# Optimization experiments

Measured on AMD Instinct MI355X. Metric: run time of the kernel, lower is better.

## Reference

```python
import jax, jax.numpy as jnp
import numpy as np

EPS = 1e-5
TAU = 0.5
K = 1024  # number of gumbel-softmax iterations


def _bn(x, gamma, beta):
    # BatchNorm1d, training semantics: batch mean, biased variance
    mean = jnp.mean(x, axis=0)
    var = jnp.mean(jnp.square(x - mean), axis=0)
    xn = (x - mean) * jax.lax.rsqrt(var + EPS)
    if gamma is None:
        return xn
    return xn * gamma + beta


def setup_inputs() -> dict:
    key = jax.random.key(0)
    ks = jax.random.split(key, 5)
    B, D, M = 64, 2048, 8192
    f = jax.random.normal(ks[0], (B, D), jnp.float32)
    W1 = jax.random.normal(ks[1], (D, M), jnp.float32) * 0.02
    b1 = jnp.zeros((M,), jnp.float32)
    g1 = jnp.ones((M,), jnp.float32)
    be1 = jnp.zeros((M,), jnp.float32)
    W2 = jax.random.normal(ks[2], (M, M), jnp.float32) * 0.02
    b2 = jnp.zeros((M,), jnp.float32)
    g2 = jnp.ones((M,), jnp.float32)
    be2 = jnp.zeros((M,), jnp.float32)
    W3 = jax.random.normal(ks[3], (M, D), jnp.float32) * 0.02
    b3 = jnp.zeros((D,), jnp.float32)
    return dict(f=f, W1=W1, b1=b1, g1=g1, be1=be1,
                W2=W2, b2=b2, g2=g2, be2=be2, W3=W3, b3=b3)


def reference(f, W1, b1, g1, be1, W2, b2, g2, be2, W3, b3):
    # MLP trunk (dropout layers are identity in eval mode)
    h = jax.nn.relu(_bn(f @ W1 + b1, g1, be1))
    h = jax.nn.relu(_bn(h @ W2 + b2, g2, be2))
    mask0 = _bn(h @ W3 + b3, None, None)  # final BN, affine=False

    noise_key = jax.random.key(42)

    def step(carry, i):
        mask, z = carry
        g = jax.random.gumbel(jax.random.fold_in(noise_key, i),
                              mask.shape, mask.dtype)
        mask = jax.nn.softmax((mask + g) / TAU, axis=1)
        z = jnp.maximum(mask, z)
        return (mask, z), None

    (_, z), _ = jax.lax.scan(step, (mask0, jnp.zeros_like(mask0)),
                             jnp.arange(K))
    return z
```

## Files before the change

kernel.cpp:

```cpp
#include <hip/hip_runtime.h>


typedef _Float16 half8 __attribute__((ext_vector_type(8)));
typedef float floatx4 __attribute__((ext_vector_type(4)));

#define TINYF 1.17549435e-38f
#define LN2F  0.69314718055994531f
#define C2F   2.8853900817779268f
#define TSCALE 512.0f
#define TS_MIN 6.11e-5f

#define COMBINE(o0, o1) ((o0) ^ (o1))

#if __has_builtin(__builtin_amdgcn_exp2f)
#define EXP2F(x) __builtin_amdgcn_exp2f(x)
#else
#define EXP2F(x) exp2f(x)
#endif
#if __has_builtin(__builtin_amdgcn_logf)
#define LOG2F(x) __builtin_amdgcn_logf(x)
#else
#define LOG2F(x) __log2f(x)
#endif
#if __has_builtin(__builtin_amdgcn_rcpf)
#define RCPF(x) __builtin_amdgcn_rcpf(x)
#else
#define RCPF(x) (1.0f/(x))
#endif

__device__ __forceinline__ unsigned rotl32(unsigned x, int r) {
  return (x << r) | (x >> (32 - r));
}

__device__ __forceinline__ void tf2x32(unsigned k0, unsigned k1,
                                       unsigned x0, unsigned x1,
                                       unsigned &o0, unsigned &o1) {
  unsigned kx = k0 ^ k1 ^ 0x1BD11BDAu;
#define TFR(r) { x0 += x1; x1 = rotl32(x1, (r)); x1 ^= x0; }
  x0 += k0; x1 += k1;
  TFR(13) TFR(15) TFR(26) TFR(6)
  x0 += k1; x1 += kx + 1u;
  TFR(17) TFR(29) TFR(16) TFR(24)
  x0 += kx; x1 += k0 + 2u;
  TFR(13) TFR(15) TFR(26) TFR(6)
  x0 += k0; x1 += k1 + 3u;
  TFR(17) TFR(29) TFR(16) TFR(24)
  x0 += k1; x1 += kx + 4u;
  TFR(13) TFR(15) TFR(26) TFR(6)
  x0 += kx; x1 += k0 + 5u;
#undef TFR
  o0 = x0; o1 = x1;
}

__device__ __forceinline__ float bits_to_t(unsigned bits) {
  float f = __uint_as_float((bits >> 9) | 0x3f800000u) - 1.0f;
  float u = fmaxf(TINYF, f + TINYF);
  return fmaxf(-LN2F * LOG2F(u), 1.0e-7f);
}

__device__ __forceinline__ float wave_sum64(float x) {
  x += __int_as_float(__builtin_amdgcn_update_dpp(0, __float_as_int(x), 0xB1, 0xF, 0xF, true));
  x += __int_as_float(__builtin_amdgcn_update_dpp(0, __float_as_int(x), 0x4E, 0xF, 0xF, true));
  x += __int_as_float(__builtin_amdgcn_update_dpp(0, __float_as_int(x), 0x141, 0xF, 0xF, true));
  x += __int_as_float(__builtin_amdgcn_update_dpp(0, __float_as_int(x), 0x140, 0xF, 0xF, true));
  x += __int_as_float(__builtin_amdgcn_update_dpp(0, __float_as_int(x), 0x142, 0xA, 0xF, true));
  x += __int_as_float(__builtin_amdgcn_update_dpp(0, __float_as_int(x), 0x143, 0xC, 0xF, true));
  return __int_as_float(__builtin_amdgcn_readlane(__float_as_int(x), 63));
}

__global__ void keys_kernel(unsigned* __restrict__ keys) {
  int i = threadIdx.x;
  unsigned o0, o1;
  tf2x32(0u, 42u, 0u, (unsigned)i, o0, o1);
  keys[2*i] = o0; keys[2*i+1] = o1;
}

__global__ void cast_kernel(const float* __restrict__ f, _Float16* __restrict__ o) {
  int i = blockIdx.x * 256 + threadIdx.x;
  o[i] = (_Float16)f[i];
}

__global__ __launch_bounds__(256) void gemm_kernel(
    const _Float16* __restrict__ A, const float* __restrict__ W,
    float* __restrict__ P, int K, int N, int KC) {
  __shared__ _Float16 As[64 * 40];
  __shared__ _Float16 Ws[128 * 40];
  const int t = threadIdx.x;
  const int lane = t & 63, w = t >> 6;
  const int c0 = blockIdx.x * 128;
  const int k0beg = blockIdx.y * KC, k0end = k0beg + KC;

  floatx4 acc[4][2];
#pragma unroll
  for (int i = 0; i < 4; ++i)
#pragma unroll
    for (int j = 0; j < 2; ++j) acc[i][j] = (floatx4){0.f, 0.f, 0.f, 0.f};

  const int ar = t >> 2;
  const int ako = (t & 3) * 8;
  const int wn = (t & 31) * 4;
  const int wk = (t >> 5) * 2;

  uint4 av = *(const uint4*)(A + (size_t)ar * K + k0beg + ako);
  float4 wv[2][2];
#pragma unroll
  for (int kk = 0; kk < 2; ++kk) {
    int krow = k0beg + kk * 16 + wk;
    wv[kk][0] = *(const float4*)(W + (size_t)krow * N + c0 + wn);
    wv[kk][1] = *(const float4*)(W + (size_t)(krow + 1) * N + c0 + wn);
  }

  for (int k0 = k0beg; k0 < k0end; k0 += 32) {
    __syncthreads();
    *(uint4*)(&As[ar * 40 + ako]) = av;
#pragma unroll
    for (int kk = 0; kk < 2; ++kk) {
#pragma unroll
      for (int i = 0; i < 4; ++i) {
        const float* p0 = (const float*)&wv[kk][0];
        const float* p1 = (const float*)&wv[kk][1];
        _Float16 h0 = (_Float16)p0[i], h1 = (_Float16)p1[i];
        unsigned u = (unsigned)*(unsigned short*)&h0 |
                     ((unsigned)*(unsigned short*)&h1 << 16);
        *(unsigned*)(&Ws[(wn + i) * 40 + kk * 16 + wk]) = u;
      }
    }
    int kn = k0 + 32;
    if (kn < k0end) {
      av = *(const uint4*)(A + (size_t)ar * K + kn + ako);
#pragma unroll
      for (int kk = 0; kk < 2; ++kk) {
        int krow = kn + kk * 16 + wk;
        wv[kk][0] = *(const float4*)(W + (size_t)krow * N + c0 + wn);
        wv[kk][1] = *(const float4*)(W + (size_t)(krow + 1) * N + c0 + wn);
      }
    }
    __syncthreads();
    const int q = lane >> 4, ml = lane & 15;
    half8 bfrag[2];
#pragma unroll
    for (int nt = 0; nt < 2; ++nt)
      bfrag[nt] = *(const half8*)(&Ws[(w * 32 + nt * 16 + ml) * 40 + q * 8]);
#pragma unroll
    for (int mt = 0; mt < 4; ++mt) {
      half8 afrag = *(const half8*)(&As[(mt * 16 + ml) * 40 + q * 8]);
      acc[mt][0] = __builtin_amdgcn_mfma_f32_16x16x32_f16(afrag, bfrag[0], acc[mt][0], 0, 0, 0);
      acc[mt][1] = __builtin_amdgcn_mfma_f32_16x16x32_f16(afrag, bfrag[1], acc[mt][1], 0, 0, 0);
    }
  }
  const int q = lane >> 4, ml = lane & 15;
  float* Pb = P + (size_t)blockIdx.y * 64 * N;
#pragma unroll
  for (int mt = 0; mt < 4; ++mt)
#pragma unroll
    for (int nt = 0; nt < 2; ++nt)
#pragma unroll
      for (int i = 0; i < 4; ++i) {
        int m = mt * 16 + q * 4 + i;
        int n = c0 + w * 32 + nt * 16 + ml;
        Pb[(size_t)m * N + n] = acc[mt][nt][i];
      }
}

__global__ __launch_bounds__(256) void reduce_kernel(
    const float* __restrict__ P, float* __restrict__ X, int nkc, int total) {
  int i = blockIdx.x * 256 + threadIdx.x;
  float s = 0.f;
  for (int kc = 0; kc < nkc; ++kc) s += P[(size_t)kc * total + i];
  X[i] = s;
}

__global__ __launch_bounds__(256) void bn_kernel(
    const float* __restrict__ P, int nkc, int N,
    const float* __restrict__ g, const float* __restrict__ be,
    _Float16* __restrict__ Hout, float* __restrict__ Fout, int mode) {
  int c = blockIdx.x * 256 + threadIdx.x;
  float x[64];
#pragma unroll
  for (int r = 0; r < 64; ++r) x[r] = 0.f;
  for (int kc = 0; kc < nkc; ++kc) {
    const float* Pb = P + (size_t)kc * 64 * N + c;
#pragma unroll
    for (int r = 0; r < 64; ++r) x[r] += Pb[(size_t)r * N];
  }
  float s = 0.f;
#pragma unroll
  for (int r = 0; r < 64; ++r) s += x[r];
  float mean = s * 0.015625f;
  float v = 0.f;
#pragma unroll
  for (int r = 0; r < 64; ++r) { float d = x[r] - mean; v += d * d; }
  v *= 0.015625f;
  float rs = rsqrtf(v + 1e-5f);
  if (mode == 0) {
    float gg = g[c], bb = be[c];
#pragma unroll
    for (int r = 0; r < 64; ++r) {
      float y = (x[r] - mean) * rs * gg + bb;
      Hout[(size_t)r * N + c] = (_Float16)fmaxf(y, 0.f);
    }
  } else {
#pragma unroll
    for (int r = 0; r < 64; ++r)
      Fout[(size_t)r * N + c] = (x[r] - mean) * rs;
  }
}

__global__ __launch_bounds__(256) void noise_kernel(
    const unsigned* __restrict__ keys, _Float16* __restrict__ noise) {
  const int bx = blockIdx.x;
  const int r = bx & 63, sg = bx >> 6;
  const int t = threadIdx.x;
  union Pack { unsigned v[16]; unsigned short us[32]; } pa;
#pragma unroll
  for (int j = 0; j < 4; ++j) {
    unsigned kk0 = keys[(sg * 4 + j) * 2];
    unsigned kk1 = keys[(sg * 4 + j) * 2 + 1];
#pragma unroll
    for (int q = 0; q < 8; ++q) {
      unsigned x1 = (unsigned)(r * 2048 + t * 8 + q);
      unsigned o0, o1;
      tf2x32(kk0, kk1, 0u, x1, o0, o1);
      float ts = fmaxf(bits_to_t(COMBINE(o0, o1)) * TSCALE, TS_MIN);
      _Float16 h = (_Float16)ts;
      pa.us[q * 4 + j] = *(unsigned short*)&h;
    }
  }
  size_t base = (((size_t)r * 256 + sg) * 2048 + (size_t)t * 8) * 4;
  uint4* wp = (uint4*)(noise + base);
#pragma unroll
  for (int i = 0; i < 4; ++i) wp[i] = ((uint4*)pa.v)[i];
}

template <int MODE>
__global__ __launch_bounds__(256) void loop_kernel(
    const float* __restrict__ mask0, const _Float16* __restrict__ noise,
    const unsigned* __restrict__ keys, float* __restrict__ zout) {
  const int row = blockIdx.x;
  const int t = threadIdx.x;
  const int lane = t & 63, w = t >> 6;
  __shared__ __align__(16) float partial[2][4];
  __shared__ unsigned keysLds[2048];

  float p[8], z[8];
  {
    union { float4 v[2]; float f[8]; } mm;
    mm.v[0] = *(const float4*)(mask0 + row * 2048 + t * 8);
    mm.v[1] = *(const float4*)(mask0 + row * 2048 + t * 8 + 4);
#pragma unroll
    for (int q = 0; q < 8; ++q) { p[q] = mm.f[q]; z[q] = 0.f; }
  }

  if (MODE == 0) {
    const _Float16* nbase = noise + (size_t)row * 2097152;
    float aC = C2F;
    float lgA[8][4], lgB[8][4];
    uint4 nbufA[4], nbufB[4];

    auto prep8 = [&](float (&LN)[8][4], const uint4 (&nbC)[4], int j) {
#pragma unroll
      for (int q = 0; q < 8; ++q) {
        int h = q * 4 + j;
        unsigned d = ((const unsigned*)&nbC[h >> 3])[(h >> 1) & 3];
        unsigned short usv = (h & 1) ? (unsigned short)(d >> 16)
                                     : (unsigned short)(d & 0xffffu);
        _Float16 hv;
        __builtin_memcpy(&hv, &usv, 2);
        LN[q][j] = -2.0f * LOG2F((float)hv);
      }
    };

    {
      uint4 nbI[4];
      const uint4* p0 = (const uint4*)(nbase + (size_t)t * 32);
      nbI[0] = p0[0]; nbI[1] = p0[1]; nbI[2] = p0[2]; nbI[3] = p0[3];
#pragma unroll
      for (int j = 0; j < 4; ++j) prep8(lgA, nbI, j);
      const uint4* p1 = (const uint4*)(nbase + 8192 + (size_t)t * 32);
      nbufA[0] = p1[0]; nbufA[1] = p1[1]; nbufA[2] = p1[2]; nbufA[3] = p1[3];
    }

    auto run_group = [&](const float (&LC)[8][4], float (&LN)[8][4],
                         const uint4 (&nbC)[4], uint4 (&nbL)[4], int sg) {
      int gl = (sg + 2 < 256) ? sg + 2 : 255;
      const uint4* pl = (const uint4*)(nbase + (size_t)gl * 8192 + (size_t)t * 32);
      nbL[0] = pl[0]; nbL[1] = pl[1]; nbL[2] = pl[2]; nbL[3] = pl[3];
#pragma unroll
      for (int j = 0; j < 4; ++j) {
        float pn[8];
#pragma unroll
        for (int q = 0; q < 8; ++q)
          pn[q] = EXP2F(fmaf(p[q], aC, LC[q][j]));
        float s = ((pn[0] + pn[1]) + (pn[2] + pn[3])) +
                  ((pn[4] + pn[5]) + (pn[6] + pn[7]));
        s = wave_sum64(s);
        if (lane == 0) partial[j & 1][w] = s;
        __syncthreads();
        float4 ps = *(const float4*)(&partial[j & 1][0]);
        prep8(LN, nbC, j);
        float S = (ps.x + ps.y) + (ps.z + ps.w);
        float inv = RCPF(S);
        aC = inv * C2F;
#pragma unroll
        for (int q = 0; q < 8; ++q) {
          z[q] = fmaxf(z[q], pn[q] * inv);
          p[q] = pn[q];
        }
      }
    };

    for (int sgp = 0; sgp < 128; ++sgp) {
      run_group(lgA, lgB, nbufA, nbufB, 2 * sgp);
      run_group(lgB, lgA, nbufB, nbufA, 2 * sgp + 1);
    }
  } else {
    for (int i = t; i < 2048; i += 256) keysLds[i] = keys[i];
    __syncthreads();
    float m[8];
#pragma unroll
    for (int q = 0; q < 8; ++q) m[q] = p[q];
    const unsigned idx0 = (unsigned)(row * 2048 + t * 8);
    for (int sg = 0; sg < 256; ++sg) {
      float rg[8][4];
#pragma unroll
      for (int j = 0; j < 4; ++j) {
        unsigned kk0 = keysLds[(sg * 4 + j) * 2];
        unsigned kk1 = keysLds[(sg * 4 + j) * 2 + 1];
#pragma unroll
        for (int q = 0; q < 8; ++q) {
          unsigned o0, o1;
          tf2x32(kk0, kk1, 0u, idx0 + q, o0, o1);
          float tt = bits_to_t(COMBINE(o0, o1));
          rg[q][j] = RCPF(tt * tt);
        }
      }
#pragma unroll
      for (int j = 0; j < 4; ++j) {
        float pp[8], loc = 0.f;
#pragma unroll
        for (int q = 0; q < 8; ++q) {
          pp[q] = EXP2F(m[q] * C2F) * rg[q][j];
          loc += pp[q];
        }
        loc = wave_sum64(loc);
        if (lane == 0) partial[j & 1][w] = loc;
        __syncthreads();
        float4 ps = *(const float4*)(&partial[j & 1][0]);
        float S = (ps.x + ps.y) + (ps.z + ps.w);
        float inv = RCPF(S);
#pragma unroll
        for (int q = 0; q < 8; ++q) {
          m[q] = pp[q] * inv;
          z[q] = fmaxf(z[q], m[q]);
        }
      }
    }
  }
  union { float4 v[2]; float f[8]; } oo;
#pragma unroll
  for (int q = 0; q < 8; ++q) oo.f[q] = z[q];
  *(float4*)(zout + row * 2048 + t * 8) = oo.v[0];
  *(float4*)(zout + row * 2048 + t * 8 + 4) = oo.v[1];
}

#define OFF_A0  65536u
#define OFF_H1  327680u
#define OFF_H2  1376256u
#define OFF_M0  2424832u
#define OFF_P   2949120u
#define OFF_XR  19726336u
#define OFF_NOISE 33554432ull
#define NEED_PRE (33554432ull + 268435456ull)

extern "C" void kernel_launch(void* const* d_in, const int* in_sizes, int n_in,
                              void* d_out, int out_size, void* d_ws, size_t ws_size,
                              hipStream_t stream) {
  const float* f   = (const float*)d_in[0];
  const float* W1  = (const float*)d_in[1];
  const float* g1  = (const float*)d_in[3];
  const float* be1 = (const float*)d_in[4];
  const float* W2  = (const float*)d_in[5];
  const float* g2  = (const float*)d_in[7];
  const float* be2 = (const float*)d_in[8];
  const float* W3  = (const float*)d_in[9];

  char* ws = (char*)d_ws;
  unsigned*  keys  = (unsigned*)(ws);
  _Float16*  A0    = (_Float16*)(ws + OFF_A0);
  _Float16*  H1    = (_Float16*)(ws + OFF_H1);
  _Float16*  H2    = (_Float16*)(ws + OFF_H2);
  float*     M0    = (float*)(ws + OFF_M0);
  float*     P     = (float*)(ws + OFF_P);
  float*     Xr    = (float*)(ws + OFF_XR);
  _Float16*  noise = (_Float16*)(ws + OFF_NOISE);
  float*     z     = (float*)d_out;
  bool pre = ws_size >= NEED_PRE;

  keys_kernel<<<1, 1024, 0, stream>>>(keys);
  cast_kernel<<<512, 256, 0, stream>>>(f, A0);
  gemm_kernel<<<dim3(64, 4), 256, 0, stream>>>(A0, W1, P, 2048, 8192, 512);
  bn_kernel<<<32, 256, 0, stream>>>(P, 4, 8192, g1, be1, H1, nullptr, 0);
  gemm_kernel<<<dim3(64, 4), 256, 0, stream>>>(H1, W2, P, 8192, 8192, 2048);
  bn_kernel<<<32, 256, 0, stream>>>(P, 4, 8192, g2, be2, H2, nullptr, 0);
  gemm_kernel<<<dim3(16, 16), 256, 0, stream>>>(H2, W3, P, 8192, 2048, 512);
  reduce_kernel<<<512, 256, 0, stream>>>(P, Xr, 16, 131072);
  bn_kernel<<<8, 256, 0, stream>>>(Xr, 1, 2048, nullptr, nullptr, nullptr, M0, 1);
  if (pre) {
    noise_kernel<<<16384, 256, 0, stream>>>(keys, noise);
    loop_kernel<0><<<64, 256, 0, stream>>>(M0, noise, keys, z);
  } else {
    loop_kernel<1><<<64, 256, 0, stream>>>(M0, nullptr, keys, z);
  }
}
```

Baseline: 1.116 ms.

## Overlap gumbel noise generation with the softmax loop across staged kernels

The single noise pre-generation pass followed by a serial 64-block loop is replaced by a staged pipeline. Each stage kernel runs the 64 row-loop blocks over one range of iteration groups while 192 extra blocks generate noise for the next range, and loop state (p, z, scale) is checkpointed to workspace between launches. The aim is to hide noise-generation time behind the latency-bound loop, which leaves most CUs idle. The cost is extra launches, state round-trips through memory, and possible interference between producer and consumer blocks on shared CUs.

Measured after the change: 1.045 ms. 1.07x faster.

```diff
diff --git a/kernel.cpp b/kernel.cpp
--- a/kernel.cpp
+++ b/kernel.cpp
@@ -206,153 +206,213 @@
   }
 }
 
+__device__ __forceinline__ void produce_gr(
+    const unsigned* __restrict__ keys, _Float16* __restrict__ noise,
+    int r, int sg, int t) {
+  unsigned k0[4], k1[4];
+#pragma unroll
+  for (int j = 0; j < 4; ++j) {
+    k0[j] = keys[(sg * 4 + j) * 2];
+    k1[j] = keys[(sg * 4 + j) * 2 + 1];
+  }
+  const unsigned bx1 = (unsigned)(r * 2048 + t * 8);
+  uint4 out[4];
+  unsigned* ow = (unsigned*)out;
+#pragma unroll
+  for (int w = 0; w < 16; ++w) {
+    const int q = w >> 1;
+    const int j = (w & 1) * 2;
+    unsigned o0, o1;
+    tf2x32(k0[j], k1[j], 0u, bx1 + (unsigned)q, o0, o1);
+    float ts0 = fmaxf(bits_to_t(COMBINE(o0, o1)) * TSCALE, TS_MIN);
+    tf2x32(k0[j + 1], k1[j + 1], 0u, bx1 + (unsigned)q, o0, o1);
+    float ts1 = fmaxf(bits_to_t(COMBINE(o0, o1)) * TSCALE, TS_MIN);
+    _Float16 h0 = (_Float16)ts0, h1 = (_Float16)ts1;
+    unsigned short u0, u1;
+    __builtin_memcpy(&u0, &h0, 2);
+    __builtin_memcpy(&u1, &h1, 2);
+    ow[w] = (unsigned)u0 | ((unsigned)u1 << 16);
+  }
+  size_t base = (((size_t)r * 256 + sg) * 2048 + (size_t)t * 8) * 4;
+  uint4* wp = (uint4*)(noise + base);
+#pragma unroll
+  for (int i = 0; i < 4; ++i) wp[i] = out[i];
+}
+
 __global__ __launch_bounds__(256) void noise_kernel(
     const unsigned* __restrict__ keys, _Float16* __restrict__ noise) {
   const int bx = blockIdx.x;
-  const int r = bx & 63, sg = bx >> 6;
+  produce_gr(keys, noise, bx & 63, bx >> 6, threadIdx.x);
+}
+
+__global__ __launch_bounds__(256) void stage_kernel(
+    const float* __restrict__ mask0, _Float16* __restrict__ noise,
+    const unsigned* __restrict__ keys, float* __restrict__ zout,
+    float* __restrict__ PST, float* __restrict__ ZST, float* __restrict__ ACR,
+    int gB, int gE, int pB, int pE) {
+  __shared__ __align__(16) float partial[2][4];
   const int t = threadIdx.x;
-  union Pack { unsigned v[16]; unsigned short us[32]; } pa;
-#pragma unroll
-  for (int j = 0; j < 4; ++j) {
-    unsigned kk0 = keys[(sg * 4 + j) * 2];
-    unsigned kk1 = keys[(sg * 4 + j) * 2 + 1];
+
+  if (blockIdx.x >= 64) {
+    const int cid = blockIdx.x - 64;
+    for (int idx = pB * 64 + cid; idx < pE * 64; idx += 192)
+      produce_gr(keys, noise, idx & 63, idx >> 6, t);
+    return;
+  }
+
+  const int row = blockIdx.x;
+  const int lane = t & 63, w = t >> 6;
+  const bool first = (gB == 0), last = (gE == 256);
+
+  float p[8], z[8];
+  if (first) {
+    union { float4 v[2]; float f[8]; } mm;
+    mm.v[0] = *(const float4*)(mask0 + row * 2048 + t * 8);
+    mm.v[1] = *(const float4*)(mask0 + row * 2048 + t * 8 + 4);
+#pragma unroll
+    for (int q = 0; q < 8; ++q) { p[q] = mm.f[q]; z[q] = 0.f; }
+  } else {
+    union { float4 v[2]; float f[8]; } mp, mz;
+    mp.v[0] = *(const float4*)(PST + row * 2048 + t * 8);
+    mp.v[1] = *(const float4*)(PST + row * 2048 + t * 8 + 4);
+    mz.v[0] = *(const float4*)(ZST + row * 2048 + t * 8);
+    mz.v[1] = *(const float4*)(ZST + row * 2048 + t * 8 + 4);
+#pragma unroll
+    for (int q = 0; q < 8; ++q) { p[q] = mp.f[q]; z[q] = mz.f[q]; }
+  }
+  float aC = first ? C2F : ACR[row];
+
+  const _Float16* nbase = noise + (size_t)row * 2097152;
+  float lgA[8][4], lgB[8][4];
+  uint4 nbufA[4], nbufB[4];
+
+  auto prep8 = [&](float (&LN)[8][4], const uint4 (&nbC)[4], int j) {
 #pragma unroll
     for (int q = 0; q < 8; ++q) {
-      unsigned x1 = (unsigned)(r * 2048 + t * 8 + q);
-      unsigned o0, o1;
-      tf2x32(kk0, kk1, 0u, x1, o0, o1);
-      float ts = fmaxf(bits_to_t(COMBINE(o0, o1)) * TSCALE, TS_MIN);
-      _Float16 h = (_Float16)ts;
-      pa.us[q * 4 + j] = *(unsigned short*)&h;
-    }
-  }
-  size_t base = (((size_t)r * 256 + sg) * 2048 + (size_t)t * 8) * 4;
-  uint4* wp = (uint4*)(noise + base);
-#pragma unroll
-  for (int i = 0; i < 4; ++i) wp[i] = ((uint4*)pa.v)[i];
-}
-
-template <int MODE>
-__global__ __launch_bounds__(256) void loop_kernel(
-    const float* __restrict__ mask0, const _Float16* __restrict__ noise,
-    const unsigned* __restrict__ keys, float* __restrict__ zout) {
+      int h = q * 4 + j;
+      unsigned d = ((const unsigned*)&nbC[h >> 3])[(h >> 1) & 3];
+      unsigned short usv = (h & 1) ? (unsigned short)(d >> 16)
+                                   : (unsigned short)(d & 0xffffu);
+      _Float16 hv;
+      __builtin_memcpy(&hv, &usv, 2);
+      LN[q][j] = -2.0f * LOG2F((float)hv);
+    }
+  };
+
+  {
+    uint4 nbI[4];
+    const uint4* p0 = (const uint4*)(nbase + (size_t)gB * 8192 + (size_t)t * 32);
+    nbI[0] = p0[0]; nbI[1] = p0[1]; nbI[2] = p0[2]; nbI[3] = p0[3];
+#pragma unroll
+    for (int j = 0; j < 4; ++j) prep8(lgA, nbI, j);
+    const uint4* p1 = (const uint4*)(nbase + (size_t)(gB + 1) * 8192 + (size_t)t * 32);
+    nbufA[0] = p1[0]; nbufA[1] = p1[1]; nbufA[2] = p1[2]; nbufA[3] = p1[3];
+  }
+
+  auto run_group = [&](const float (&LC)[8][4], float (&LN)[8][4],
+                       const uint4 (&nbC)[4], uint4 (&nbL)[4], int sg) {
+    int gl = (sg + 2 < gE) ? sg + 2 : gE - 1;
+    const uint4* pl = (const uint4*)(nbase + (size_t)gl * 8192 + (size_t)t * 32);
+    nbL[0] = pl[0]; nbL[1] = pl[1]; nbL[2] = pl[2]; nbL[3] = pl[3];
+#pragma unroll
+    for (int j = 0; j < 4; ++j) {
+      float pn[8];
+#pragma unroll
+      for (int q = 0; q < 8; ++q)
+        pn[q] = EXP2F(fmaf(p[q], aC, LC[q][j]));
+      float s = ((pn[0] + pn[1]) + (pn[2] + pn[3])) +
+                ((pn[4] + pn[5]) + (pn[6] + pn[7]));
+      s = wave_sum64(s);
+      if (lane == 0) partial[j & 1][w] = s;
+      __syncthreads();
+      float4 ps = *(const float4*)(&partial[j & 1][0]);
+      prep8(LN, nbC, j);
+      float S = (ps.x + ps.y) + (ps.z + ps.w);
+      float inv = RCPF(S);
+      aC = inv * C2F;
+#pragma unroll
+      for (int q = 0; q < 8; ++q) {
+        z[q] = fmaxf(z[q], pn[q] * inv);
+        p[q] = pn[q];
+      }
+    }
+  };
+
+  for (int sg = gB; sg < gE; sg += 2) {
+    run_group(lgA, lgB, nbufA, nbufB, sg);
+    run_group(lgB, lgA, nbufB, nbufA, sg + 1);
+  }
+
+  if (last) {
+    union { float4 v[2]; float f[8]; } oo;
+#pragma unroll
+    for (int q = 0; q < 8; ++q) oo.f[q] = z[q];
+    *(float4*)(zout + row * 2048 + t * 8) = oo.v[0];
+    *(float4*)(zout + row * 2048 + t * 8 + 4) = oo.v[1];
+  } else {
+    union { float4 v[2]; float f[8]; } op, oz;
+#pragma unroll
+    for (int q = 0; q < 8; ++q) { op.f[q] = p[q]; oz.f[q] = z[q]; }
+    *(float4*)(PST + row * 2048 + t * 8) = op.v[0];
+    *(float4*)(PST + row * 2048 + t * 8 + 4) = op.v[1];
+    *(float4*)(ZST + row * 2048 + t * 8) = oz.v[0];
+    *(float4*)(ZST + row * 2048 + t * 8 + 4) = oz.v[1];
+    if (t == 0) ACR[row] = aC;
+  }
+}
+
+__global__ __launch_bounds__(256) void loop_fallback_kernel(
+    const float* __restrict__ mask0, const unsigned* __restrict__ keys,
+    float* __restrict__ zout) {
   const int row = blockIdx.x;
   const int t = threadIdx.x;
   const int lane = t & 63, w = t >> 6;
   __shared__ __align__(16) float partial[2][4];
   __shared__ unsigned keysLds[2048];
 
-  float p[8], z[8];
+  float m[8], z[8];
   {
     union { float4 v[2]; float f[8]; } mm;
     mm.v[0] = *(const float4*)(mask0 + row * 2048 + t * 8);
     mm.v[1] = *(const float4*)(mask0 + row * 2048 + t * 8 + 4);
 #pragma unroll
-    for (int q = 0; q < 8; ++q) { p[q] = mm.f[q]; z[q] = 0.f; }
-  }
-
-  if (MODE == 0) {
-    const _Float16* nbase = noise + (size_t)row * 2097152;
-    float aC = C2F;
-    float lgA[8][4], lgB[8][4];
-    uint4 nbufA[4], nbufB[4];
-
-    auto prep8 = [&](float (&LN)[8][4], const uint4 (&nbC)[4], int j) {
+    for (int q = 0; q < 8; ++q) { m[q] = mm.f[q]; z[q] = 0.f; }
+  }
+  for (int i = t; i < 2048; i += 256) keysLds[i] = keys[i];
+  __syncthreads();
+  const unsigned idx0 = (unsigned)(row * 2048 + t * 8);
+  for (int sg = 0; sg < 256; ++sg) {
+    float rg[8][4];
+#pragma unroll
+    for (int j = 0; j < 4; ++j) {
+      unsigned kk0 = keysLds[(sg * 4 + j) * 2];
+      unsigned kk1 = keysLds[(sg * 4 + j) * 2 + 1];
 #pragma unroll
       for (int q = 0; q < 8; ++q) {
-        int h = q * 4 + j;
-        unsigned d = ((const unsigned*)&nbC[h >> 3])[(h >> 1) & 3];
-        unsigned short usv = (h & 1) ? (unsigned short)(d >> 16)
-                                     : (unsigned short)(d & 0xffffu);
-        _Float16 hv;
-        __builtin_memcpy(&hv, &usv, 2);
-        LN[q][j] = -2.0f * LOG2F((float)hv);
-      }
-    };
-
-    {
-      uint4 nbI[4];
-      const uint4* p0 = (const uint4*)(nbase + (size_t)t * 32);
-      nbI[0] = p0[0]; nbI[1] = p0[1]; nbI[2] = p0[2]; nbI[3] = p0[3];
-#pragma unroll
-      for (int j = 0; j < 4; ++j) prep8(lgA, nbI, j);
-      const uint4* p1 = (const uint4*)(nbase + 8192 + (size_t)t * 32);
-      nbufA[0] = p1[0]; nbufA[1] = p1[1]; nbufA[2] = p1[2]; nbufA[3] = p1[3];
-    }
-
-    auto run_group = [&](const float (&LC)[8][4], float (&LN)[8][4],
-                         const uint4 (&nbC)[4], uint4 (&nbL)[4], int sg) {
-      int gl = (sg + 2 < 256) ? sg + 2 : 255;
-      const uint4* pl = (const uint4*)(nbase + (size_t)gl * 8192 + (size_t)t * 32);
-      nbL[0] = pl[0]; nbL[1] = pl[1]; nbL[2] = pl[2]; nbL[3] = pl[3];
-#pragma unroll
-      for (int j = 0; j < 4; ++j) {
-        float pn[8];
-#pragma unroll
-        for (int q = 0; q < 8; ++q)
-          pn[q] = EXP2F(fmaf(p[q], aC, LC[q][j]));
-        float s = ((pn[0] + pn[1]) + (pn[2] + pn[3])) +
-                  ((pn[4] + pn[5]) + (pn[6] + pn[7]));
-        s = wave_sum64(s);
-        if (lane == 0) partial[j & 1][w] = s;
-        __syncthreads();
-        float4 ps = *(const float4*)(&partial[j & 1][0]);
-        prep8(LN, nbC, j);
-        float S = (ps.x + ps.y) + (ps.z + ps.w);
-        float inv = RCPF(S);
-        aC = inv * C2F;
-#pragma unroll
-        for (int q = 0; q < 8; ++q) {
-          z[q] = fmaxf(z[q], pn[q] * inv);
-          p[q] = pn[q];
-        }
-      }
-    };
-
-    for (int sgp = 0; sgp < 128; ++sgp) {
-      run_group(lgA, lgB, nbufA, nbufB, 2 * sgp);
-      run_group(lgB, lgA, nbufB, nbufA, 2 * sgp + 1);
-    }
-  } else {
-    for (int i = t; i < 2048; i += 256) keysLds[i] = keys[i];
-    __syncthreads();
-    float m[8];
-#pragma unroll
-    for (int q = 0; q < 8; ++q) m[q] = p[q];
-    const unsigned idx0 = (unsigned)(row * 2048 + t * 8);
-    for (int sg = 0; sg < 256; ++sg) {
-      float rg[8][4];
-#pragma unroll
-      for (int j = 0; j < 4; ++j) {
-        unsigned kk0 = keysLds[(sg * 4 + j) * 2];
-        unsigned kk1 = keysLds[(sg * 4 + j) * 2 + 1];
-#pragma unroll
-        for (int q = 0; q < 8; ++q) {
-          unsigned o0, o1;
-          tf2x32(kk0, kk1, 0u, idx0 + q, o0, o1);
-          float tt = bits_to_t(COMBINE(o0, o1));
-          rg[q][j] = RCPF(tt * tt);
-        }
-      }
-#pragma unroll
-      for (int j = 0; j < 4; ++j) {
-        float pp[8], loc = 0.f;
-#pragma unroll
-        for (int q = 0; q < 8; ++q) {
-          pp[q] = EXP2F(m[q] * C2F) * rg[q][j];
-          loc += pp[q];
-        }
-        loc = wave_sum64(loc);
-        if (lane == 0) partial[j & 1][w] = loc;
-        __syncthreads();
-        float4 ps = *(const float4*)(&partial[j & 1][0]);
-        float S = (ps.x + ps.y) + (ps.z + ps.w);
-        float inv = RCPF(S);
-#pragma unroll
-        for (int q = 0; q < 8; ++q) {
-          m[q] = pp[q] * inv;
-          z[q] = fmaxf(z[q], m[q]);
-        }
+        unsigned o0, o1;
+        tf2x32(kk0, kk1, 0u, idx0 + q, o0, o1);
+        float tt = bits_to_t(COMBINE(o0, o1));
+        rg[q][j] = RCPF(tt * tt);
+      }
+    }
+#pragma unroll
+    for (int j = 0; j < 4; ++j) {
+      float pp[8], loc = 0.f;
+#pragma unroll
+      for (int q = 0; q < 8; ++q) {
+        pp[q] = EXP2F(m[q] * C2F) * rg[q][j];
+        loc += pp[q];
+      }
+      loc = wave_sum64(loc);
+      if (lane == 0) partial[j & 1][w] = loc;
+      __syncthreads();
+      float4 ps = *(const float4*)(&partial[j & 1][0]);
+      float S = (ps.x + ps.y) + (ps.z + ps.w);
+      float inv = RCPF(S);
+#pragma unroll
+      for (int q = 0; q < 8; ++q) {
+        m[q] = pp[q] * inv;
+        z[q] = fmaxf(z[q], m[q]);
       }
     }
   }
@@ -369,6 +429,9 @@
 #define OFF_M0  2424832u
 #define OFF_P   2949120u
 #define OFF_XR  19726336u
+#define OFF_PST 20971520u
+#define OFF_ZST 21495808u
+#define OFF_ACR 22020096u
 #define OFF_NOISE 33554432ull
 #define NEED_PRE (33554432ull + 268435456ull)
 
@@ -392,6 +455,9 @@
   float*     M0    = (float*)(ws + OFF_M0);
   float*     P     = (float*)(ws + OFF_P);
   float*     Xr    = (float*)(ws + OFF_XR);
+  float*     PST   = (float*)(ws + OFF_PST);
+  float*     ZST   = (float*)(ws + OFF_ZST);
+  float*     ACR   = (float*)(ws + OFF_ACR);
   _Float16*  noise = (_Float16*)(ws + OFF_NOISE);
   float*     z     = (float*)d_out;
   bool pre = ws_size >= NEED_PRE;
@@ -406,9 +472,16 @@
   reduce_kernel<<<512, 256, 0, stream>>>(P, Xr, 16, 131072);
   bn_kernel<<<8, 256, 0, stream>>>(Xr, 1, 2048, nullptr, nullptr, nullptr, M0, 1);
   if (pre) {
-    noise_kernel<<<16384, 256, 0, stream>>>(keys, noise);
-    loop_kernel<0><<<64, 256, 0, stream>>>(M0, noise, keys, z);
+    noise_kernel<<<40 * 64, 256, 0, stream>>>(keys, noise);
+    stage_kernel<<<256, 256, 0, stream>>>(M0, noise, keys, z, PST, ZST, ACR,
+                                          0, 40, 40, 104);
+    stage_kernel<<<256, 256, 0, stream>>>(M0, noise, keys, z, PST, ZST, ACR,
+                                          40, 104, 104, 200);
+    stage_kernel<<<256, 256, 0, stream>>>(M0, noise, keys, z, PST, ZST, ACR,
+                                          104, 200, 200, 256);
+    stage_kernel<<<64, 256, 0, stream>>>(M0, noise, keys, z, PST, ZST, ACR,
+                                         200, 256, 256, 256);
   } else {
-    loop_kernel<1><<<64, 256, 0, stream>>>(M0, nullptr, keys, z);
-  }
-}
+    loop_fallback_kernel<<<64, 256, 0, stream>>>(M0, keys, z);
+  }
+}
```
